# Optimization experiments

Hardware: AMD Instinct MI355X
Metric: run time of the kernel (lower is better)

## Reference

```python
import jax, jax.numpy as jnp
import numpy as np

IN_C = 1
BASE_C = 16
N3, N2, N1 = 262144, 65536, 16384

def _quadconv(feat, neigh, w, b):
    # feat: [N, C]; neigh: [N, 9] with -1 padding -> gather via extra zero row
    N = feat.shape[0]
    feat_p = jnp.concatenate([feat, jnp.zeros((1, feat.shape[1]), feat.dtype)], axis=0)
    gidx = jnp.where(neigh == -1, N, neigh)
    col = feat_p[gidx].reshape(N, -1)  # [N, 9*C] im2col
    return col @ w.T + b

def _parent_idx(keys, parent_keys):
    return jnp.searchsorted(parent_keys, keys >> 2)

def _quadpool(feat, keys, parent_keys):
    pidx = _parent_idx(keys, parent_keys)
    p = jax.ops.segment_max(feat, pidx, num_segments=parent_keys.shape[0])
    # original inits with -1e9 and zeroes untouched slots; segment_max uses -inf fill
    return jnp.where(jnp.isneginf(p), jnp.zeros((), feat.dtype), p), pidx

def _quadunpool(feat, keys, parent_keys):
    return feat[_parent_idx(keys, parent_keys)]

def _lin(key, out_f, in_f, scale=0.05):
    kw, kb = jax.random.split(key)
    return (jax.random.normal(kw, (out_f, in_f), jnp.float32) * scale,
            jnp.zeros((out_f,), jnp.float32))

def setup_inputs() -> dict:
    key = jax.random.key(0)
    ks = jax.random.split(key, 12)
    inp = {
        'features': jax.random.normal(ks[0], (N3, IN_C), jnp.float32),
        'keys3': jnp.arange(N3, dtype=jnp.int32),
        'keys2': jnp.arange(N2, dtype=jnp.int32),
        'keys1': jnp.arange(N1, dtype=jnp.int32),
        'neighs3': jax.random.randint(ks[1], (N3, 9), -1, N3, jnp.int32),
        'neighs2': jax.random.randint(ks[2], (N2, 9), -1, N2, jnp.int32),
        'neighs1': jax.random.randint(ks[3], (N1, 9), -1, N1, jnp.int32),
    }
    c = BASE_C
    inp['w_enc1'], inp['b_enc1'] = _lin(ks[4], c, 9 * IN_C)
    inp['w_enc2'], inp['b_enc2'] = _lin(ks[5], 2 * c, 9 * c)
    inp['w_enc3'], inp['b_enc3'] = _lin(ks[6], 4 * c, 9 * 2 * c)
    inp['w_dec1'], inp['b_dec1'] = _lin(ks[7], 2 * c, 9 * 4 * c)
    inp['w_dec2'], inp['b_dec2'] = _lin(ks[8], c, 9 * 2 * c)
    inp['w_head'], inp['b_head'] = _lin(ks[9], IN_C, 9 * c)
    return inp

def reference(features, keys3, keys2, keys1, neighs3, neighs2, neighs1,
              w_enc1, b_enc1, w_enc2, b_enc2, w_enc3, b_enc3,
              w_dec1, b_dec1, w_dec2, b_dec2, w_head, b_head):
    relu = jax.nn.relu
    x8 = relu(_quadconv(features, neighs3, w_enc1, b_enc1))
    x7_p, _ = _quadpool(x8, keys3, keys2)
    x7 = relu(_quadconv(x7_p, neighs2, w_enc2, b_enc2))
    x6_p, _ = _quadpool(x7, keys2, keys1)
    x6 = relu(_quadconv(x6_p, neighs1, w_enc3, b_enc3))
    x7_up = _quadunpool(x6, keys2, keys1)
    x7_dec = relu(_quadconv(x7_up, neighs2, w_dec1, b_dec1))
    x8_up = _quadunpool(x7_dec, keys3, keys2)
    x8_dec = relu(_quadconv(x8_up, neighs3, w_dec2, b_dec2))
    return _quadconv(x8_dec, neighs3, w_head, b_head)
```

## Files before the change

### kernel.cpp

```cpp
#include <hip/hip_runtime.h>
#include <stdint.h>

#define NN3 262144
#define NN2 65536
#define NN1 16384

typedef __attribute__((ext_vector_type(8))) __bf16 bf16x8;
typedef __attribute__((ext_vector_type(4))) float floatx4;
typedef __attribute__((ext_vector_type(4))) unsigned int uint4v;

static __device__ __forceinline__ float bf2f(unsigned short u) {
    union { unsigned int i; float f; } v; v.i = ((unsigned int)u) << 16; return v.f;
}
static __device__ __forceinline__ unsigned short f2bf(float f) {
    union { float f; unsigned int i; } v; v.f = f;
    unsigned int x = v.i;
    return (unsigned short)((x + 0x7fffu + ((x >> 16) & 1u)) >> 16);
}
static __device__ __forceinline__ bf16x8 zero_bf16x8() {
    bf16x8 z;
#pragma unroll
    for (int i = 0; i < 8; ++i) z[i] = (__bf16)0.0f;
    return z;
}

__global__ __launch_bounds__(256) void enc1pool_kernel(
    const float* __restrict__ feat, const int* __restrict__ neigh,
    const float* __restrict__ w, const float* __restrict__ b,
    unsigned short* __restrict__ x7p,
    const float* __restrict__ w_enc2, const float* __restrict__ w_enc3,
    const float* __restrict__ w_dec1, const float* __restrict__ w_dec2,
    unsigned short* __restrict__ wb_enc2, unsigned short* __restrict__ wb_enc3,
    unsigned short* __restrict__ wb_dec1, unsigned short* __restrict__ wb_dec2)
{
    {
        int g = blockIdx.x * 256 + threadIdx.x;
        if (g < 4608) wb_enc2[g] = f2bf(w_enc2[g]);
        else {
            g -= 4608;
            if (g < 18432) wb_enc3[g] = f2bf(w_enc3[g]);
            else {
                g -= 18432;
                if (g < 18432) wb_dec1[g] = f2bf(w_dec1[g]);
                else { g -= 18432; if (g < 4608) wb_dec2[g] = f2bf(w_dec2[g]); }
            }
        }
    }
    __shared__ float wsf[4][160];
    __shared__ int nsh[4][576];
    int t = threadIdx.x;
    int lane = t & 63, wave = t >> 6;
    int wbase = blockIdx.x * 256 + wave * 64;
    for (int e = lane; e < 160; e += 64) wsf[wave][e] = (e < 144) ? w[e] : b[e - 144];
    for (int e = lane; e < 576; e += 64)
        nsh[wave][e] = __builtin_nontemporal_load(&neigh[(size_t)wbase * 9 + e]);
    __builtin_amdgcn_wave_barrier();
    float f[9];
#pragma unroll
    for (int k = 0; k < 9; ++k) { int j = nsh[wave][lane * 9 + k]; f[k] = (j < 0) ? 0.0f : feat[j]; }
    float v[16];
#pragma unroll
    for (int co = 0; co < 16; ++co) {
        float a = wsf[wave][144 + co];
#pragma unroll
        for (int k = 0; k < 9; ++k) a += f[k] * wsf[wave][co * 9 + k];
        v[co] = fmaxf(a, 0.0f);
    }
#pragma unroll
    for (int co = 0; co < 16; ++co) {
        v[co] = fmaxf(v[co], __shfl_xor(v[co], 1));
        v[co] = fmaxf(v[co], __shfl_xor(v[co], 2));
    }
    if ((lane & 3) == 0) {
        uint4v o0, o1;
#pragma unroll
        for (int h = 0; h < 4; ++h)
            o0[h] = (unsigned int)f2bf(v[2 * h]) | (((unsigned int)f2bf(v[2 * h + 1])) << 16);
#pragma unroll
        for (int h = 0; h < 4; ++h)
            o1[h] = (unsigned int)f2bf(v[8 + 2 * h]) | (((unsigned int)f2bf(v[9 + 2 * h])) << 16);
        uint4v* dst = (uint4v*)(x7p + (size_t)((wbase + lane) >> 2) * 16);
        __builtin_nontemporal_store(o0, &dst[0]);
        __builtin_nontemporal_store(o1, &dst[1]);
    }
}

template <int CIN, int COUT, bool SHIFT, bool POOL, int TILES>
__global__ __launch_bounds__(256) void conv_mfma(
    const unsigned short* __restrict__ src, const int* __restrict__ neigh,
    const unsigned short* __restrict__ wb, const float* __restrict__ bias,
    unsigned short* __restrict__ dst)
{
    constexpr int K  = 9 * CIN;
    constexpr int KT = (K + 31) / 32;
    constexpr int NT = COUT / 16;
    constexpr int LSTRIDE = COUT + 8;
    __shared__ int nsh[4][TILES * 144];
    __shared__ __align__(16) unsigned short tsh[4][16 * LSTRIDE];
    int t = threadIdx.x;
    int lane = t & 63, wave = t >> 6;
    int rowbase = blockIdx.x * (64 * TILES);
#pragma unroll
    for (int tl = 0; tl < TILES; ++tl) {
        const int* srcn = &neigh[(size_t)(rowbase + tl * 64 + wave * 16) * 9];
        for (int e = lane; e < 144; e += 64) {
            int j = __builtin_nontemporal_load(&srcn[e]);
            if (SHIFT) j = (j < 0) ? -1 : (j >> 2);
            nsh[wave][tl * 144 + e] = j;
        }
    }
    __builtin_amdgcn_wave_barrier();
    int m    = lane & 15;
    int quad = lane >> 4;
    floatx4 acc[TILES][NT];
#pragma unroll
    for (int tl = 0; tl < TILES; ++tl)
#pragma unroll
        for (int n = 0; n < NT; ++n) acc[tl][n] = (floatx4){0.f, 0.f, 0.f, 0.f};
    for (int kt = 0; kt < KT; ++kt) {
        int k0 = kt * 32 + quad * 8;
        bf16x8 a[TILES];
#pragma unroll
        for (int tl = 0; tl < TILES; ++tl) {
            a[tl] = zero_bf16x8();
            if (k0 < K) {
                int nb = k0 / CIN;
                int ci = k0 % CIN;
                int j  = nsh[wave][tl * 144 + m * 9 + nb];
                if (j >= 0) a[tl] = *(const bf16x8*)(src + (size_t)j * CIN + ci);
            }
        }
#pragma unroll
        for (int n = 0; n < NT; ++n) {
            bf16x8 bfrag = zero_bf16x8();
            if (k0 < K) bfrag = *(const bf16x8*)(wb + (size_t)(n * 16 + m) * K + k0);
#pragma unroll
            for (int tl = 0; tl < TILES; ++tl)
                acc[tl][n] = __builtin_amdgcn_mfma_f32_16x16x32_bf16(a[tl], bfrag, acc[tl][n], 0, 0, 0);
        }
    }
#pragma unroll
    for (int tl = 0; tl < TILES; ++tl) {
        int tbase = rowbase + tl * 64;
        if (POOL) {
            int p = (tbase >> 2) + wave * 4 + quad;
#pragma unroll
            for (int n = 0; n < NT; ++n) {
                int cout = n * 16 + m;
                float vm = fmaxf(fmaxf(acc[tl][n][0], acc[tl][n][1]), fmaxf(acc[tl][n][2], acc[tl][n][3]));
                float v  = fmaxf(vm + bias[cout], 0.0f);
                __builtin_nontemporal_store(f2bf(v), &dst[(size_t)p * COUT + cout]);
            }
        } else {
#pragma unroll
            for (int n = 0; n < NT; ++n) {
                int cout = n * 16 + m;
                float bv = bias[cout];
#pragma unroll
                for (int r = 0; r < 4; ++r) {
                    float v = fmaxf(acc[tl][n][r] + bv, 0.0f);
                    tsh[wave][(quad * 4 + r) * LSTRIDE + cout] = f2bf(v);
                }
            }
            __builtin_amdgcn_wave_barrier();
            constexpr int CPR = COUT / 8;
            constexpr int CHUNKS = 16 * CPR;
            int wrow = tbase + wave * 16;
#pragma unroll
            for (int c = lane; c < CHUNKS; c += 64) {
                int row = c / CPR;
                int ch  = c % CPR;
                uint4v val = *(const uint4v*)&tsh[wave][row * LSTRIDE + ch * 8];
                __builtin_nontemporal_store(val,
                    (uint4v*)&dst[(size_t)(wrow + row) * COUT + ch * 8]);
            }
            __builtin_amdgcn_wave_barrier();
        }
    }
}

static __device__ __forceinline__ float dot2(unsigned int u, const float* w) {
    return bf2f((unsigned short)(u & 0xffffu)) * w[0] + bf2f((unsigned short)(u >> 16)) * w[1];
}
__global__ __launch_bounds__(256) void head_kernel(
    const unsigned short* __restrict__ x, const int* __restrict__ neigh,
    const float* __restrict__ w, const float* __restrict__ b, float* __restrict__ out)
{
    __shared__ float wsf[4][144];
    __shared__ int nsh[4][1152];
    int t = threadIdx.x;
    int lane = t & 63, wave = t >> 6;
    int base = blockIdx.x * 512;
    int r0base = base + wave * 64;
    int r1base = base + 256 + wave * 64;
    for (int e = lane; e < 144; e += 64) wsf[wave][e] = w[e];
    for (int e = lane; e < 576; e += 64) {
        nsh[wave][e]       = __builtin_nontemporal_load(&neigh[(size_t)r0base * 9 + e]);
        nsh[wave][576 + e] = __builtin_nontemporal_load(&neigh[(size_t)r1base * 9 + e]);
    }
    __builtin_amdgcn_wave_barrier();
    float acc0 = b[0], acc1 = b[0];
#pragma unroll
    for (int k = 0; k < 9; ++k) {
        int j0 = nsh[wave][lane * 9 + k];
        int j1 = nsh[wave][576 + lane * 9 + k];
        const float* wp = &wsf[wave][k * 16];
        if (j0 >= 0) {
            const uint4v* r = (const uint4v*)(x + (size_t)j0 * 16);
            uint4v A = r[0], B = r[1];
            acc0 += dot2(A[0], wp)     + dot2(A[1], wp + 2)  + dot2(A[2], wp + 4)  + dot2(A[3], wp + 6);
            acc0 += dot2(B[0], wp + 8) + dot2(B[1], wp + 10) + dot2(B[2], wp + 12) + dot2(B[3], wp + 14);
        }
        if (j1 >= 0) {
            const uint4v* r = (const uint4v*)(x + (size_t)j1 * 16);
            uint4v A = r[0], B = r[1];
            acc1 += dot2(A[0], wp)     + dot2(A[1], wp + 2)  + dot2(A[2], wp + 4)  + dot2(A[3], wp + 6);
            acc1 += dot2(B[0], wp + 8) + dot2(B[1], wp + 10) + dot2(B[2], wp + 12) + dot2(B[3], wp + 14);
        }
    }
    __builtin_nontemporal_store(acc0, &out[r0base + lane]);
    __builtin_nontemporal_store(acc1, &out[r1base + lane]);
}

extern "C" void kernel_launch(void* const* d_in, const int* in_sizes, int n_in,
                              void* d_out, int out_size, void* d_ws, size_t ws_size,
                              hipStream_t stream) {
    const float* features = (const float*)d_in[0];
    const int* neighs3 = (const int*)d_in[4];
    const int* neighs2 = (const int*)d_in[5];
    const int* neighs1 = (const int*)d_in[6];
    const float* w_enc1 = (const float*)d_in[7];
    const float* b_enc1 = (const float*)d_in[8];
    const float* w_enc2 = (const float*)d_in[9];
    const float* b_enc2 = (const float*)d_in[10];
    const float* w_enc3 = (const float*)d_in[11];
    const float* b_enc3 = (const float*)d_in[12];
    const float* w_dec1 = (const float*)d_in[13];
    const float* b_dec1 = (const float*)d_in[14];
    const float* w_dec2 = (const float*)d_in[15];
    const float* b_dec2 = (const float*)d_in[16];
    const float* w_head = (const float*)d_in[17];
    const float* b_head = (const float*)d_in[18];

    char* ws = (char*)d_ws;
    size_t off = 0;
    unsigned short* wb_enc2 = (unsigned short*)(ws + off); off += 4608 * 2;
    unsigned short* wb_enc3 = (unsigned short*)(ws + off); off += 18432 * 2;
    unsigned short* wb_dec1 = (unsigned short*)(ws + off); off += 18432 * 2;
    unsigned short* wb_dec2 = (unsigned short*)(ws + off); off += 4608 * 2;
    unsigned short* x7p   = (unsigned short*)(ws + off); off += (size_t)NN2 * 16 * 2;
    unsigned short* x6p   = (unsigned short*)(ws + off); off += (size_t)NN1 * 32 * 2;
    unsigned short* x6    = (unsigned short*)(ws + off); off += (size_t)NN1 * 64 * 2;
    unsigned short* x7dec = (unsigned short*)(ws + off); off += (size_t)NN2 * 32 * 2;
    unsigned short* x8dec = (unsigned short*)(ws + off); off += (size_t)NN3 * 16 * 2;

    enc1pool_kernel<<<NN3 / 256, 256, 0, stream>>>(features, neighs3, w_enc1, b_enc1, x7p,
                                                   w_enc2, w_enc3, w_dec1, w_dec2,
                                                   wb_enc2, wb_enc3, wb_dec1, wb_dec2);
    conv_mfma<16, 32, false, true, 2><<<NN2 / 128, 256, 0, stream>>>(x7p, neighs2, wb_enc2, b_enc2, x6p);
    conv_mfma<32, 64, false, false, 1><<<NN1 / 64, 256, 0, stream>>>(x6p, neighs1, wb_enc3, b_enc3, x6);
    conv_mfma<64, 32, true, false, 2><<<NN2 / 128, 256, 0, stream>>>(x6, neighs2, wb_dec1, b_dec1, x7dec);
    conv_mfma<32, 16, true, false, 4><<<NN3 / 256, 256, 0, stream>>>(x7dec, neighs3, wb_dec2, b_dec2, x8dec);
    head_kernel<<<NN3 / 512, 256, 0, stream>>>(x8dec, neighs3, w_head, b_head, (float*)d_out);
}
```

Before: 202.8 us.

## Fuse middle three conv layers into one persistent kernel with grid barriers

Replaces the three separate launches for enc2 (with pooling), enc3 and dec1 with a single persistent kernel of 256 blocks. The blocks loop over 64-row units and are separated by a software grid-wide barrier built on agent-scope atomics, with the counter reset inside the first kernel. This is meant to remove kernel launch gaps and tail effects on the small middle layers. In exchange it gives up the multi-tile register reuse of the old kernels, and it depends on all 256 blocks being co-resident, since otherwise the barrier deadlocks.

Measured after the change: 253.4 us. 1.25x slower.

```diff
diff --git a/kernel.cpp b/kernel.cpp
--- a/kernel.cpp
+++ b/kernel.cpp
@@ -22,6 +22,24 @@
 #pragma unroll
     for (int i = 0; i < 8; ++i) z[i] = (__bf16)0.0f;
     return z;
+}
+
+static __device__ __forceinline__ void grid_barrier(int* cnt, int* gen) {
+    __syncthreads();
+    if (threadIdx.x == 0) {
+        __builtin_amdgcn_fence(__ATOMIC_RELEASE, "agent");
+        int g = __hip_atomic_load(gen, __ATOMIC_RELAXED, __HIP_MEMORY_SCOPE_AGENT);
+        int prev = __hip_atomic_fetch_add(cnt, 1, __ATOMIC_RELAXED, __HIP_MEMORY_SCOPE_AGENT);
+        if (prev == (int)gridDim.x - 1) {
+            __hip_atomic_store(cnt, 0, __ATOMIC_RELAXED, __HIP_MEMORY_SCOPE_AGENT);
+            __hip_atomic_store(gen, g + 1, __ATOMIC_RELAXED, __HIP_MEMORY_SCOPE_AGENT);
+        } else {
+            while (__hip_atomic_load(gen, __ATOMIC_RELAXED, __HIP_MEMORY_SCOPE_AGENT) == g)
+                __builtin_amdgcn_s_sleep(1);
+        }
+        __builtin_amdgcn_fence(__ATOMIC_ACQUIRE, "agent");
+    }
+    __syncthreads();
 }
 
 __global__ __launch_bounds__(256) void enc1pool_kernel(
@@ -31,8 +49,10 @@
     const float* __restrict__ w_enc2, const float* __restrict__ w_enc3,
     const float* __restrict__ w_dec1, const float* __restrict__ w_dec2,
     unsigned short* __restrict__ wb_enc2, unsigned short* __restrict__ wb_enc3,
-    unsigned short* __restrict__ wb_dec1, unsigned short* __restrict__ wb_dec2)
-{
+    unsigned short* __restrict__ wb_dec1, unsigned short* __restrict__ wb_dec2,
+    int* __restrict__ bar)
+{
+    if (blockIdx.x == 0 && threadIdx.x == 0) { bar[0] = 0; bar[16] = 0; }
     {
         int g = blockIdx.x * 256 + threadIdx.x;
         if (g < 4608) wb_enc2[g] = f2bf(w_enc2[g]);
@@ -85,7 +105,106 @@
     }
 }
 
-template <int CIN, int COUT, bool SHIFT, bool POOL, int TILES>
+template <int CIN, int COUT, bool SHIFT, bool POOL>
+static __device__ __forceinline__ void conv_unit(
+    const unsigned short* __restrict__ src, const int* __restrict__ neigh,
+    const unsigned short* __restrict__ wb, const float* __restrict__ bias,
+    unsigned short* __restrict__ dst, int* nshw, unsigned short* tshw,
+    int unit, int lane, int wave)
+{
+    constexpr int K  = 9 * CIN;
+    constexpr int KT = (K + 31) / 32;
+    constexpr int NT = COUT / 16;
+    constexpr int LSTRIDE = COUT + 8;
+    int rowbase = unit * 64;
+    const int* srcn = &neigh[(size_t)(rowbase + wave * 16) * 9];
+    for (int e = lane; e < 144; e += 64) {
+        int j = __builtin_nontemporal_load(&srcn[e]);
+        if (SHIFT) j = (j < 0) ? -1 : (j >> 2);
+        nshw[e] = j;
+    }
+    __builtin_amdgcn_wave_barrier();
+    int m = lane & 15, quad = lane >> 4;
+    floatx4 acc[NT];
+#pragma unroll
+    for (int n = 0; n < NT; ++n) acc[n] = (floatx4){0.f, 0.f, 0.f, 0.f};
+#pragma unroll
+    for (int kt = 0; kt < KT; ++kt) {
+        int k0 = kt * 32 + quad * 8;
+        bf16x8 a = zero_bf16x8();
+        if (k0 < K) {
+            int nb = k0 / CIN;
+            int ci = k0 % CIN;
+            int j  = nshw[m * 9 + nb];
+            if (j >= 0) a = *(const bf16x8*)(src + (size_t)j * CIN + ci);
+        }
+#pragma unroll
+        for (int n = 0; n < NT; ++n) {
+            bf16x8 bfrag = zero_bf16x8();
+            if (k0 < K) bfrag = *(const bf16x8*)(wb + (size_t)(n * 16 + m) * K + k0);
+            acc[n] = __builtin_amdgcn_mfma_f32_16x16x32_bf16(a, bfrag, acc[n], 0, 0, 0);
+        }
+    }
+    if (POOL) {
+        int p = (rowbase >> 2) + wave * 4 + quad;
+#pragma unroll
+        for (int n = 0; n < NT; ++n) {
+            int cout = n * 16 + m;
+            float vm = fmaxf(fmaxf(acc[n][0], acc[n][1]), fmaxf(acc[n][2], acc[n][3]));
+            float v  = fmaxf(vm + bias[cout], 0.0f);
+            __builtin_nontemporal_store(f2bf(v), &dst[(size_t)p * COUT + cout]);
+        }
+    } else {
+#pragma unroll
+        for (int n = 0; n < NT; ++n) {
+            int cout = n * 16 + m;
+            float bv = bias[cout];
+#pragma unroll
+            for (int r = 0; r < 4; ++r) {
+                float v = fmaxf(acc[n][r] + bv, 0.0f);
+                tshw[(quad * 4 + r) * LSTRIDE + cout] = f2bf(v);
+            }
+        }
+        __builtin_amdgcn_wave_barrier();
+        constexpr int CPR = COUT / 8;
+        constexpr int CHUNKS = 16 * CPR;
+        int wrow = rowbase + wave * 16;
+#pragma unroll
+        for (int c = lane; c < CHUNKS; c += 64) {
+            int row = c / CPR;
+            int ch  = c % CPR;
+            uint4v val = *(const uint4v*)&tshw[row * LSTRIDE + ch * 8];
+            __builtin_nontemporal_store(val,
+                (uint4v*)&dst[(size_t)(wrow + row) * COUT + ch * 8]);
+        }
+        __builtin_amdgcn_wave_barrier();
+    }
+}
+
+__global__ __launch_bounds__(256) void mid_kernel(
+    const unsigned short* __restrict__ x7p, const int* __restrict__ n2, const int* __restrict__ n1,
+    const unsigned short* __restrict__ wb_enc2, const float* __restrict__ b_enc2,
+    unsigned short* __restrict__ x6p,
+    const unsigned short* __restrict__ wb_enc3, const float* __restrict__ b_enc3,
+    unsigned short* __restrict__ x6,
+    const unsigned short* __restrict__ wb_dec1, const float* __restrict__ b_dec1,
+    unsigned short* __restrict__ x7dec,
+    int* __restrict__ bar)
+{
+    __shared__ int nsh[4][144];
+    __shared__ __align__(16) unsigned short tsh[4][16 * 72];
+    int t = threadIdx.x, lane = t & 63, wave = t >> 6;
+    for (int u = blockIdx.x; u < NN2 / 64; u += 256)
+        conv_unit<16, 32, false, true>(x7p, n2, wb_enc2, b_enc2, x6p, nsh[wave], tsh[wave], u, lane, wave);
+    grid_barrier(bar, bar + 16);
+    for (int u = blockIdx.x; u < NN1 / 64; u += 256)
+        conv_unit<32, 64, false, false>(x6p, n1, wb_enc3, b_enc3, x6, nsh[wave], tsh[wave], u, lane, wave);
+    grid_barrier(bar, bar + 16);
+    for (int u = blockIdx.x; u < NN2 / 64; u += 256)
+        conv_unit<64, 32, true, false>(x6, n2, wb_dec1, b_dec1, x7dec, nsh[wave], tsh[wave], u, lane, wave);
+}
+
+template <int CIN, int COUT, bool SHIFT, int TILES>
 __global__ __launch_bounds__(256) void conv_mfma(
     const unsigned short* __restrict__ src, const int* __restrict__ neigh,
     const unsigned short* __restrict__ wb, const float* __restrict__ bias,
@@ -142,40 +261,29 @@
 #pragma unroll
     for (int tl = 0; tl < TILES; ++tl) {
         int tbase = rowbase + tl * 64;
-        if (POOL) {
-            int p = (tbase >> 2) + wave * 4 + quad;
-#pragma unroll
-            for (int n = 0; n < NT; ++n) {
-                int cout = n * 16 + m;
-                float vm = fmaxf(fmaxf(acc[tl][n][0], acc[tl][n][1]), fmaxf(acc[tl][n][2], acc[tl][n][3]));
-                float v  = fmaxf(vm + bias[cout], 0.0f);
-                __builtin_nontemporal_store(f2bf(v), &dst[(size_t)p * COUT + cout]);
+#pragma unroll
+        for (int n = 0; n < NT; ++n) {
+            int cout = n * 16 + m;
+            float bv = bias[cout];
+#pragma unroll
+            for (int r = 0; r < 4; ++r) {
+                float v = fmaxf(acc[tl][n][r] + bv, 0.0f);
+                tsh[wave][(quad * 4 + r) * LSTRIDE + cout] = f2bf(v);
             }
-        } else {
-#pragma unroll
-            for (int n = 0; n < NT; ++n) {
-                int cout = n * 16 + m;
-                float bv = bias[cout];
-#pragma unroll
-                for (int r = 0; r < 4; ++r) {
-                    float v = fmaxf(acc[tl][n][r] + bv, 0.0f);
-                    tsh[wave][(quad * 4 + r) * LSTRIDE + cout] = f2bf(v);
-                }
-            }
-            __builtin_amdgcn_wave_barrier();
-            constexpr int CPR = COUT / 8;
-            constexpr int CHUNKS = 16 * CPR;
-            int wrow = tbase + wave * 16;
-#pragma unroll
-            for (int c = lane; c < CHUNKS; c += 64) {
-                int row = c / CPR;
-                int ch  = c % CPR;
-                uint4v val = *(const uint4v*)&tsh[wave][row * LSTRIDE + ch * 8];
-                __builtin_nontemporal_store(val,
-                    (uint4v*)&dst[(size_t)(wrow + row) * COUT + ch * 8]);
-            }
-            __builtin_amdgcn_wave_barrier();
-        }
+        }
+        __builtin_amdgcn_wave_barrier();
+        constexpr int CPR = COUT / 8;
+        constexpr int CHUNKS = 16 * CPR;
+        int wrow = tbase + wave * 16;
+#pragma unroll
+        for (int c = lane; c < CHUNKS; c += 64) {
+            int row = c / CPR;
+            int ch  = c % CPR;
+            uint4v val = *(const uint4v*)&tsh[wave][row * LSTRIDE + ch * 8];
+            __builtin_nontemporal_store(val,
+                (uint4v*)&dst[(size_t)(wrow + row) * COUT + ch * 8]);
+        }
+        __builtin_amdgcn_wave_barrier();
     }
 }
 
@@ -244,6 +352,7 @@
 
     char* ws = (char*)d_ws;
     size_t off = 0;
+    int* bar = (int*)(ws + off); off += 256;
     unsigned short* wb_enc2 = (unsigned short*)(ws + off); off += 4608 * 2;
     unsigned short* wb_enc3 = (unsigned short*)(ws + off); off += 18432 * 2;
     unsigned short* wb_dec1 = (unsigned short*)(ws + off); off += 18432 * 2;
@@ -256,10 +365,11 @@
 
     enc1pool_kernel<<<NN3 / 256, 256, 0, stream>>>(features, neighs3, w_enc1, b_enc1, x7p,
                                                    w_enc2, w_enc3, w_dec1, w_dec2,
-                                                   wb_enc2, wb_enc3, wb_dec1, wb_dec2);
-    conv_mfma<16, 32, false, true, 2><<<NN2 / 128, 256, 0, stream>>>(x7p, neighs2, wb_enc2, b_enc2, x6p);
-    conv_mfma<32, 64, false, false, 1><<<NN1 / 64, 256, 0, stream>>>(x6p, neighs1, wb_enc3, b_enc3, x6);
-    conv_mfma<64, 32, true, false, 2><<<NN2 / 128, 256, 0, stream>>>(x6, neighs2, wb_dec1, b_dec1, x7dec);
-    conv_mfma<32, 16, true, false, 4><<<NN3 / 256, 256, 0, stream>>>(x7dec, neighs3, wb_dec2, b_dec2, x8dec);
+                                                   wb_enc2, wb_enc3, wb_dec1, wb_dec2, bar);
+    mid_kernel<<<256, 256, 0, stream>>>(x7p, neighs2, neighs1,
+                                        wb_enc2, b_enc2, x6p,
+                                        wb_enc3, b_enc3, x6,
+                                        wb_dec1, b_dec1, x7dec, bar);
+    conv_mfma<32, 16, true, 4><<<NN3 / 256, 256, 0, stream>>>(x7dec, neighs3, wb_dec2, b_dec2, x8dec);
     head_kernel<<<NN3 / 512, 256, 0, stream>>>(x8dec, neighs3, w_head, b_head, (float*)d_out);
 }
```
